# Optimization experiments

Measured on AMD Instinct MI355X. Metric: run time of the kernel, lower is better.

The kernel has to match this reference:

```python
import jax, jax.numpy as jnp
import numpy as np

NUM_HEADS = 12
WH, WW = 14, 14
NUM_REL = (2 * WH - 1) * (2 * WW - 1) + 3  # 732


def binarize(x):
    # STESign forward: sign(x) with sign(0) -> +1
    return jnp.where(x >= 0, 1.0, -1.0).astype(x.dtype)


def quantize_qk(x):
    # per-(B,H) scale: mean |x| over token and feature dims
    s = jnp.mean(jnp.abs(x), axis=(-2, -1), keepdims=True)
    return s * binarize(x)


def quantize_p(x):
    qmax = 255.0
    s = 1.0 / qmax
    q = jnp.clip(jnp.round(x / s), 0.0, qmax)
    return s * q


def symquantize_v(x, num_bits=8):
    # SymQuantizer, layerwise=False: per-column max over dim=-2
    m = jnp.max(jnp.abs(x), axis=-2, keepdims=True)
    s = (2.0 ** (num_bits - 1) - 1.0) / (m + 1e-6)
    return jnp.round(x * s) / (s + 1e-6)


def make_rel_index():
    coords = np.stack(np.meshgrid(np.arange(WH), np.arange(WW), indexing='ij'))  # [2,Wh,Ww]
    flat = coords.reshape(2, -1)                                                 # [2,Wh*Ww]
    rel = flat[:, :, None] - flat[:, None, :]                                    # [2,N-1,N-1]
    rel = rel.transpose(1, 2, 0).copy()
    rel[:, :, 0] += WH - 1
    rel[:, :, 1] += WW - 1
    rel[:, :, 0] *= 2 * WW - 1
    n = WH * WW + 1
    idx = np.zeros((n, n), dtype=np.int64)
    idx[1:, 1:] = rel.sum(-1)
    idx[0, :] = NUM_REL - 3
    idx[:, 0] = NUM_REL - 2
    idx[0, 0] = NUM_REL - 1
    return idx


def setup_inputs() -> dict:
    key = jax.random.key(0)
    k1, k2, k3, k4 = jax.random.split(key, 4)
    B, N, C = 64, WH * WW + 1, 768
    x = jax.random.normal(k1, (B, N, C), dtype=jnp.float32)
    w_qkv = jax.random.normal(k2, (3 * C, C), dtype=jnp.float32) * 0.02
    w_proj = jax.random.normal(k3, (C, C), dtype=jnp.float32) * 0.02
    b_proj = jnp.zeros((C,), dtype=jnp.float32)
    rpb_table = jax.random.normal(k4, (NUM_REL, NUM_HEADS), dtype=jnp.float32) * 0.02
    rel_index = jnp.asarray(make_rel_index())
    return {"x": x, "w_qkv": w_qkv, "w_proj": w_proj, "b_proj": b_proj,
            "rpb_table": rpb_table, "rel_index": rel_index}


def reference(x, w_qkv, w_proj, b_proj, rpb_table, rel_index):
    B, N, C = x.shape
    H = NUM_HEADS
    D = C // H
    scale = D ** (-0.5)
    qkv = (x @ w_qkv.T).reshape(B, N, 3, H, D)
    qkv = jnp.transpose(qkv, (2, 0, 3, 1, 4))  # [3,B,H,N,D]
    q, k, v = qkv[0], qkv[1], qkv[2]
    q = quantize_qk(q)
    k = quantize_qk(k)
    attn = jnp.einsum('bhnd,bhmd->bhnm', q, k) * scale
    bias = rpb_table[rel_index]                 # [N,N,H]
    attn = attn + jnp.transpose(bias, (2, 0, 1))[None]  # [1,H,N,N]
    attn = jax.nn.softmax(attn, axis=-1)
    attn = quantize_p(attn)
    v = symquantize_v(v, 8)
    out = jnp.einsum('bhnm,bhmd->bhnd', attn, v)
    out = jnp.transpose(out, (0, 2, 1, 3)).reshape(B, N, C)
    return out @ w_proj.T + b_proj
```

## Files before the change

### kernel.cpp

```cpp
#include <hip/hip_runtime.h>
#include <hip/hip_bf16.h>
#include <math.h>

#define NUM_HEADS 12
#define N_TOK 197
#define C_DIM 768
#define B_SZ 64
#define M_ROWS (B_SZ * N_TOK)
#define QKV_COLS (3 * C_DIM)
#define NN (N_TOK * N_TOK)
#define VT_PITCH 232

#define MPAD 12800
#define APLANE ((size_t)MPAD * C_DIM)
#define BPLANE ((size_t)QKV_COLS * C_DIM)
#define NT6 144

typedef __hip_bfloat16 bf16;
typedef __attribute__((ext_vector_type(8))) short short8;
typedef __attribute__((ext_vector_type(4))) short s16x4;
typedef __attribute__((ext_vector_type(4))) float floatx4;
typedef unsigned long long u64;

__device__ __forceinline__ void split2(float x, short& hi, short& lo) {
    bf16 h = __float2bfloat16(x);
    float hf = __bfloat162float(h);
    bf16 l = __float2bfloat16(x - hf);
    hi = __builtin_bit_cast(short, h);
    lo = __builtin_bit_cast(short, l);
}

__device__ __forceinline__ void split3(float x, short& s0, short& s1, short& s2) {
    bf16 h = __float2bfloat16(x);
    float r1 = x - __bfloat162float(h);
    bf16 m = __float2bfloat16(r1);
    float r2 = r1 - __bfloat162float(m);
    bf16 l = __float2bfloat16(r2);
    s0 = __builtin_bit_cast(short, h);
    s1 = __builtin_bit_cast(short, m);
    s2 = __builtin_bit_cast(short, l);
}

__device__ __forceinline__ void async16(const void* g, void* l) {
    __builtin_amdgcn_global_load_lds(
        (const __attribute__((address_space(1))) void*)g,
        (__attribute__((address_space(3))) void*)l,
        16, 0, 0);
}

__global__ __launch_bounds__(192) void split3_pack(
    const float* __restrict__ src, short* __restrict__ dst,
    int rows_in, size_t plane)
{
    const int row = blockIdx.x;
    const int c = threadIdx.x * 4;
    const size_t o = (size_t)row * C_DIM + c;
    if (row < rows_in) {
        float4 v = *(const float4*)(src + o);
        float xs[4] = {v.x, v.y, v.z, v.w};
        s16x4 h, m, l;
#pragma unroll
        for (int e = 0; e < 4; ++e) {
            short a, b, cc; split3(xs[e], a, b, cc);
            h[e] = a; m[e] = b; l[e] = cc;
        }
        *(s16x4*)(dst + o) = h;
        *(s16x4*)(dst + plane + o) = m;
        *(s16x4*)(dst + 2 * plane + o) = l;
    } else {
        s16x4 z = (s16x4){0, 0, 0, 0};
        *(s16x4*)(dst + o) = z;
        *(s16x4*)(dst + plane + o) = z;
        *(s16x4*)(dst + 2 * plane + o) = z;
    }
}

__global__ __launch_bounds__(512, 2) void gemm6_pipe(
    const short* __restrict__ Abig, const short* __restrict__ Bbig,
    float* __restrict__ C, int M, int N)
{
    __shared__ short Abuf[4][256 * 32];
    __shared__ short Bbuf[4][256 * 32];

    const int t = threadIdx.x;
    const int wave = t >> 6, lane = t & 63;
    const int quad = lane >> 4, mrow = lane & 15;
    const int wm = wave >> 2, wn = wave & 3;

    const int old = blockIdx.x + blockIdx.y * 9;
    const int xcd = old & 7, wi = old >> 3;
    const int nid = (xcd < 2 ? xcd * 57 : 114 + (xcd - 2) * 56) + wi;
    const int tm = nid / 9;
    const int tile_m = tm * 256;
    const int tile_n = (nid - tm * 9) * 256;

    const int lrow = lane >> 2;
    const int lgp  = lane & 3;
    const int lByte = lrow * (C_DIM * 2) + ((lgp ^ ((lrow >> 1) & 3)) << 4);

    const char* Ab0 = (const char*)Abig + (size_t)(tile_m + wave * 16) * (C_DIM * 2);
    const char* Bb0 = (const char*)Bbig + (size_t)(tile_n + wave * 16) * (C_DIM * 2);

    auto stage = [&](int s) {
        if (s >= NT6) return;
        int term = s / 24;
        int k0b = (s - term * 24) * 64;
        int ta = (0x910 >> (2 * term)) & 3;
        int tb = (0x184 >> (2 * term)) & 3;
        const char* As = Ab0 + (size_t)ta * (APLANE * 2) + k0b + lByte;
        const char* Bs = Bb0 + (size_t)tb * (BPLANE * 2) + k0b + lByte;
        short* la = &Abuf[s & 3][wave * 16 * 32];
        short* lb = &Bbuf[s & 3][wave * 16 * 32];
        async16(As, la);
        async16(As + (size_t)128 * (C_DIM * 2), la + 128 * 32);
        async16(Bs, lb);
        async16(Bs + (size_t)128 * (C_DIM * 2), lb + 128 * 32);
    };

    const int gsel = (quad ^ ((mrow >> 1) & 3)) << 3;
    const int aoff = (wm * 128 + mrow) * 32 + gsel;
    const int boff = (wn * 64 + mrow) * 32 + gsel;

    floatx4 acc[8][4];
#pragma unroll
    for (int i = 0; i < 8; ++i)
#pragma unroll
        for (int j = 0; j < 4; ++j) acc[i][j] = (floatx4){0.f, 0.f, 0.f, 0.f};

    short8 afA[4], afB[4], bf0[4], bf1[4];

    stage(0); stage(1); stage(2);
    asm volatile("s_waitcnt vmcnt(8)" ::: "memory");
    asm volatile("" ::: "memory");
    __builtin_amdgcn_s_barrier();
    asm volatile("" ::: "memory");
    {
        const short* Ab = Abuf[0];
        const short* Bb = Bbuf[0];
#pragma unroll
        for (int i = 0; i < 4; ++i) afA[i] = *(const short8*)&Ab[aoff + i * 512];
#pragma unroll
        for (int j = 0; j < 4; ++j) bf0[j] = *(const short8*)&Bb[boff + j * 512];
    }

    auto iter = [&](int tt, short8 (&bc)[4], short8 (&bn)[4]) {
        const short* Ab = Abuf[tt & 3];
        stage(tt + 3);
#pragma unroll
        for (int i = 0; i < 4; ++i)
            afB[i] = *(const short8*)&Ab[aoff + (4 + i) * 512];
        __builtin_amdgcn_s_setprio(1);
#pragma unroll
        for (int i = 0; i < 4; ++i)
#pragma unroll
            for (int j = 0; j < 4; ++j)
                acc[i][j] = __builtin_amdgcn_mfma_f32_16x16x32_bf16(afA[i], bc[j], acc[i][j], 0, 0, 0);
        __builtin_amdgcn_s_setprio(0);
        if (tt < NT6 - 3) { asm volatile("s_waitcnt vmcnt(8)" ::: "memory"); }
        else              { asm volatile("s_waitcnt vmcnt(0)" ::: "memory"); }
        asm volatile("s_waitcnt lgkmcnt(0)" ::: "memory");
        asm volatile("" ::: "memory");
        __builtin_amdgcn_s_barrier();
        asm volatile("" ::: "memory");
        if (tt + 1 < NT6) {
            const short* An = Abuf[(tt + 1) & 3];
            const short* Bn = Bbuf[(tt + 1) & 3];
#pragma unroll
            for (int i = 0; i < 4; ++i) afA[i] = *(const short8*)&An[aoff + i * 512];
#pragma unroll
            for (int j = 0; j < 4; ++j) bn[j] = *(const short8*)&Bn[boff + j * 512];
        }
        __builtin_amdgcn_s_setprio(1);
#pragma unroll
        for (int i = 0; i < 4; ++i)
#pragma unroll
            for (int j = 0; j < 4; ++j)
                acc[4 + i][j] = __builtin_amdgcn_mfma_f32_16x16x32_bf16(afB[i], bc[j], acc[4 + i][j], 0, 0, 0);
        __builtin_amdgcn_s_setprio(0);
    };

    for (int kt = 0; kt < NT6; kt += 2) {
        iter(kt, bf0, bf1);
        iter(kt + 1, bf1, bf0);
    }

#pragma unroll
    for (int i = 0; i < 8; ++i)
#pragma unroll
        for (int r = 0; r < 4; ++r) {
            int grow = tile_m + wm * 128 + i * 16 + quad * 4 + r;
            if (grow < M)
#pragma unroll
                for (int j = 0; j < 4; ++j)
                    C[(size_t)grow * N + tile_n + wn * 64 + j * 16 + mrow] = acc[i][j][r];
        }
}

__global__ __launch_bounds__(256) void gemm_split6(
    const float* __restrict__ A, const float* __restrict__ B,
    float* __restrict__ C, int M, int N, int K)
{
    __shared__ short8 As[3][512];
    __shared__ short8 Bs[3][512];
    const int t = threadIdx.x;
    const int tile_m = blockIdx.y * 128;
    const int tile_n = blockIdx.x * 128;
    const int wave = t >> 6, lane = t & 63;
    const int quad = lane >> 4, mrow = lane & 15;
    const int wrow = (wave >> 1) * 64, wcol = (wave & 1) * 64;

    floatx4 acc[4][4];
#pragma unroll
    for (int i = 0; i < 4; ++i)
#pragma unroll
        for (int j = 0; j < 4; ++j) acc[i][j] = (floatx4){0.f, 0.f, 0.f, 0.f};

    for (int k0 = 0; k0 < K; k0 += 32) {
        __syncthreads();
#pragma unroll
        for (int s = 0; s < 2; ++s) {
            int idx = s * 256 + t;
            int row = idx >> 2, q = idx & 3;
            {
                int ga = tile_m + row;
                float4 a0 = {0.f, 0.f, 0.f, 0.f}, a1 = {0.f, 0.f, 0.f, 0.f};
                if (ga < M) {
                    const float* p = A + (size_t)ga * K + k0 + q * 8;
                    a0 = *(const float4*)p;
                    a1 = *(const float4*)(p + 4);
                }
                float xs[8] = {a0.x, a0.y, a0.z, a0.w, a1.x, a1.y, a1.z, a1.w};
                short8 v0, v1, v2;
#pragma unroll
                for (int e = 0; e < 8; ++e) {
                    short h, m, l; split3(xs[e], h, m, l);
                    v0[e] = h; v1[e] = m; v2[e] = l;
                }
                As[0][q * 128 + row] = v0;
                As[1][q * 128 + row] = v1;
                As[2][q * 128 + row] = v2;
            }
            {
                int gb = tile_n + row;
                float4 b0 = {0.f, 0.f, 0.f, 0.f}, b1 = {0.f, 0.f, 0.f, 0.f};
                if (gb < N) {
                    const float* p = B + (size_t)gb * K + k0 + q * 8;
                    b0 = *(const float4*)p;
                    b1 = *(const float4*)(p + 4);
                }
                float xs[8] = {b0.x, b0.y, b0.z, b0.w, b1.x, b1.y, b1.z, b1.w};
                short8 v0, v1, v2;
#pragma unroll
                for (int e = 0; e < 8; ++e) {
                    short h, m, l; split3(xs[e], h, m, l);
                    v0[e] = h; v1[e] = m; v2[e] = l;
                }
                Bs[0][q * 128 + row] = v0;
                Bs[1][q * 128 + row] = v1;
                Bs[2][q * 128 + row] = v2;
            }
        }
        __syncthreads();

        short8 af[4], bfr[4];
#pragma unroll
        for (int ta = 0; ta < 3; ++ta) {
#pragma unroll
            for (int i = 0; i < 4; ++i)
                af[i] = As[ta][quad * 128 + wrow + i * 16 + mrow];
            const int ntb = 3 - ta;
#pragma unroll
            for (int tb = 0; tb < 3; ++tb) {
                if (tb >= ntb) break;
#pragma unroll
                for (int j = 0; j < 4; ++j)
                    bfr[j] = Bs[tb][quad * 128 + wcol + j * 16 + mrow];
#pragma unroll
                for (int i = 0; i < 4; ++i)
#pragma unroll
                    for (int j = 0; j < 4; ++j)
                        acc[i][j] = __builtin_amdgcn_mfma_f32_16x16x32_bf16(af[i], bfr[j], acc[i][j], 0, 0, 0);
            }
        }
    }

#pragma unroll
    for (int i = 0; i < 4; ++i)
#pragma unroll
        for (int r = 0; r < 4; ++r) {
            int grow = tile_m + wrow + i * 16 + quad * 4 + r;
            if (grow < M)
#pragma unroll
                for (int j = 0; j < 4; ++j) {
                    int gcol = tile_n + wcol + j * 16 + mrow;
                    C[(size_t)grow * N + gcol] = acc[i][j][r];
                }
        }
}

__global__ __launch_bounds__(256) void gemm_split4_bias(
    const float* __restrict__ A, const float* __restrict__ B,
    const float* __restrict__ bias, float* __restrict__ C,
    int M, int N, int K)
{
    __shared__ short8 Ah[512], Al[512];
    __shared__ short8 Bh[512], Bl[512];
    const int t = threadIdx.x;
    const int tile_m = blockIdx.y * 128;
    const int tile_n = blockIdx.x * 128;
    const int wave = t >> 6, lane = t & 63;
    const int quad = lane >> 4, mrow = lane & 15;
    const int wrow = (wave >> 1) * 64, wcol = (wave & 1) * 64;

    floatx4 acc[4][4];
#pragma unroll
    for (int i = 0; i < 4; ++i)
#pragma unroll
        for (int j = 0; j < 4; ++j) acc[i][j] = (floatx4){0.f, 0.f, 0.f, 0.f};

    for (int k0 = 0; k0 < K; k0 += 32) {
        __syncthreads();
#pragma unroll
        for (int s = 0; s < 2; ++s) {
            int idx = s * 256 + t;
            int row = idx >> 2, q = idx & 3;
            {
                int ga = tile_m + row;
                float4 a0 = {0.f, 0.f, 0.f, 0.f}, a1 = {0.f, 0.f, 0.f, 0.f};
                if (ga < M) {
                    const float* p = A + (size_t)ga * K + k0 + q * 8;
                    a0 = *(const float4*)p; a1 = *(const float4*)(p + 4);
                }
                float xs[8] = {a0.x, a0.y, a0.z, a0.w, a1.x, a1.y, a1.z, a1.w};
                short8 hi, lo;
#pragma unroll
                for (int e = 0; e < 8; ++e) { short hh, ll; split2(xs[e], hh, ll); hi[e] = hh; lo[e] = ll; }
                Ah[q * 128 + row] = hi; Al[q * 128 + row] = lo;
            }
            {
                int gb = tile_n + row;
                float4 b0 = {0.f, 0.f, 0.f, 0.f}, b1 = {0.f, 0.f, 0.f, 0.f};
                if (gb < N) {
                    const float* p = B + (size_t)gb * K + k0 + q * 8;
                    b0 = *(const float4*)p; b1 = *(const float4*)(p + 4);
                }
                float xs[8] = {b0.x, b0.y, b0.z, b0.w, b1.x, b1.y, b1.z, b1.w};
                short8 hi, lo;
#pragma unroll
                for (int e = 0; e < 8; ++e) { short hh, ll; split2(xs[e], hh, ll); hi[e] = hh; lo[e] = ll; }
                Bh[q * 128 + row] = hi; Bl[q * 128 + row] = lo;
            }
        }
        __syncthreads();
        short8 ah[4], al[4], bh[4], bl[4];
#pragma unroll
        for (int i = 0; i < 4; ++i) {
            ah[i] = Ah[quad * 128 + wrow + i * 16 + mrow];
            al[i] = Al[quad * 128 + wrow + i * 16 + mrow];
        }
#pragma unroll
        for (int j = 0; j < 4; ++j) {
            bh[j] = Bh[quad * 128 + wcol + j * 16 + mrow];
            bl[j] = Bl[quad * 128 + wcol + j * 16 + mrow];
        }
#pragma unroll
        for (int i = 0; i < 4; ++i)
#pragma unroll
            for (int j = 0; j < 4; ++j) {
                acc[i][j] = __builtin_amdgcn_mfma_f32_16x16x32_bf16(al[i], bl[j], acc[i][j], 0, 0, 0);
                acc[i][j] = __builtin_amdgcn_mfma_f32_16x16x32_bf16(al[i], bh[j], acc[i][j], 0, 0, 0);
                acc[i][j] = __builtin_amdgcn_mfma_f32_16x16x32_bf16(ah[i], bl[j], acc[i][j], 0, 0, 0);
                acc[i][j] = __builtin_amdgcn_mfma_f32_16x16x32_bf16(ah[i], bh[j], acc[i][j], 0, 0, 0);
            }
    }

#pragma unroll
    for (int i = 0; i < 4; ++i)
#pragma unroll
        for (int r = 0; r < 4; ++r) {
            int grow = tile_m + wrow + i * 16 + quad * 4 + r;
            if (grow < M)
#pragma unroll
                for (int j = 0; j < 4; ++j) {
                    int gcol = tile_n + wcol + j * 16 + mrow;
                    C[(size_t)grow * N + gcol] = acc[i][j][r] + bias[gcol];
                }
        }
}

__global__ __launch_bounds__(256) void quant_stats(
    const float* __restrict__ qkv, float* __restrict__ sqf, float* __restrict__ skf,
    u64* __restrict__ qbits, u64* __restrict__ kbits, float* __restrict__ svf)
{
    const int bh = blockIdx.x;
    const int b = bh / NUM_HEADS, h = bh % NUM_HEADS;
    const int t = threadIdx.x;
    const size_t base = (size_t)b * N_TOK * QKV_COLS + h * 64;
    __shared__ double red[256];
    __shared__ float redf[256];

    const int d = t & 63;
    double aq = 0.0, ak = 0.0;
    for (int i = t; i < N_TOK * 64; i += 256) {
        int n = i >> 6;
        size_t off = base + (size_t)n * QKV_COLS + d;
        aq += (double)fabsf(qkv[off]);
        ak += (double)fabsf(qkv[off + C_DIM]);
    }
    red[t] = aq; __syncthreads();
    for (int s = 128; s > 0; s >>= 1) { if (t < s) red[t] += red[t + s]; __syncthreads(); }
    if (t == 0) sqf[bh] = (float)(red[0] / 12608.0);
    __syncthreads();
    red[t] = ak; __syncthreads();
    for (int s = 128; s > 0; s >>= 1) { if (t < s) red[t] += red[t + s]; __syncthreads(); }
    if (t == 0) skf[bh] = (float)(red[0] / 12608.0);
    __syncthreads();

    float vm = 0.f;
    for (int n = (t >> 6); n < N_TOK; n += 4)
        vm = fmaxf(vm, fabsf(qkv[base + (size_t)n * QKV_COLS + 2 * C_DIM + d]));
    redf[t] = vm; __syncthreads();
    if (t < 64) {
        float m4 = fmaxf(fmaxf(redf[t], redf[t + 64]), fmaxf(redf[t + 128], redf[t + 192]));
        svf[bh * 64 + t] = 127.0f / (m4 + 1e-6f);
    }

    const int wave = t >> 6, lane = t & 63;
    for (int n = wave; n < N_TOK; n += 4) {
        size_t off = base + (size_t)n * QKV_COLS + lane;
        u64 bq = __ballot(qkv[off] >= 0.f);
        u64 bk = __ballot(qkv[off + C_DIM] >= 0.f);
        if (lane == 0) { qbits[bh * N_TOK + n] = bq; kbits[bh * N_TOK + n] = bk; }
    }
}

__global__ void detect_rel64(const int* __restrict__ rel, int* __restrict__ flag)
{
    __shared__ int nz;
    if (threadIdx.x == 0) nz = 0;
    __syncthreads();
    int local = 0;
    for (int i = threadIdx.x; i < NN / 2; i += 256)
        if (rel[2 * i + 1] != 0) local = 1;
    if (local) atomicOr(&nz, 1);
    __syncthreads();
    if (threadIdx.x == 0) flag[0] = (nz == 0) ? 1 : 0;
}

__global__ void build_bias(const float* __restrict__ rpb, const int* __restrict__ rel,
                           const int* __restrict__ flag, float* __restrict__ bias_f)
{
    int nm = blockIdx.x * 256 + threadIdx.x;
    int h = blockIdx.y;
    if (nm < NN) {
        int idx = flag[0] ? rel[2 * nm] : rel[nm];
        bias_f[(size_t)h * NN + nm] = rpb[idx * NUM_HEADS + h];
    }
}

__global__ __launch_bounds__(256) void attn_mfma(
    const float* __restrict__ qkv, const float* __restrict__ sqf, const float* __restrict__ skf,
    const u64* __restrict__ qbits, const u64* __restrict__ kbits,
    const float* __restrict__ svf, const float* __restrict__ bias_f,
    float* __restrict__ attn_out)
{
    const int bh = blockIdx.x;
    const int b = bh / NUM_HEADS, h = bh % NUM_HEADS;
    const int t = threadIdx.x;
    const int wave = t >> 6, lane = t & 63;
    const int quad = lane >> 4, mrow = lane & 15;

    __shared__ __align__(16) short vth[64 * VT_PITCH];
    __shared__ __align__(16) short vtl[64 * VT_PITCH];
    __shared__ __align__(16) short pbuf[2][16 * VT_PITCH];
    __shared__ u64 qb[N_TOK], kb[N_TOK];

    for (int i = t; i < N_TOK; i += 256) {
        qb[i] = qbits[bh * N_TOK + i];
        kb[i] = kbits[bh * N_TOK + i];
    }

    const size_t vbase = (size_t)b * N_TOK * QKV_COLS + 2 * C_DIM + h * 64;
    const int d0 = t & 63;
    const float sv = svf[bh * 64 + d0];
    const float inv_sv = sv + 1e-6f;
    for (int i = t; i < N_TOK * 64; i += 256) {
        int n = i >> 6;
        float v = qkv[vbase + (size_t)n * QKV_COLS + d0];
        float vqf = rintf(v * sv) / inv_sv;
        short hh, ll; split2(vqf, hh, ll);
        vth[d0 * VT_PITCH + n] = hh;
        vtl[d0 * VT_PITCH + n] = ll;
    }
    for (int i = t; i < 64 * (VT_PITCH - N_TOK); i += 256) {
        int d = i / (VT_PITCH - N_TOK), n = N_TOK + i % (VT_PITCH - N_TOK);
        vth[d * VT_PITCH + n] = 0;
        vtl[d * VT_PITCH + n] = 0;
    }
    __syncthreads();

    const int ct = wave;
    short8 bfh[7], bfl[7];
#pragma unroll
    for (int kt = 0; kt < 7; ++kt) {
        int off = (ct * 16 + mrow) * VT_PITCH + kt * 32 + quad * 8;
        bfh[kt] = *(const short8*)&vth[off];
        bfl[kt] = *(const short8*)&vtl[off];
    }

    const float cf = sqf[bh] * skf[bh] * 0.125f;
    const float* bh_bias = bias_f + (size_t)h * NN;
    const float qs = 1.0f / 255.0f;

    auto computeP = [&](int strip, int buf) {
        short* pb = &pbuf[buf][0];
#pragma unroll
        for (int rr = 0; rr < 4; ++rr) {
            int nl = wave * 4 + rr;
            int n = strip * 16 + nl;
            short* prow = pb + nl * VT_PITCH;
            int m0 = lane, m1 = 64 + lane, m2 = 128 + lane, m3 = 192 + lane;
            if (n < N_TOK) {
                const u64 qn = qb[n];
                const float* brow = bh_bias + (size_t)n * N_TOK;
                float l0 = cf * (float)(64 - 2 * (int)__popcll(qn ^ kb[m0])) + brow[m0];
                float l1 = cf * (float)(64 - 2 * (int)__popcll(qn ^ kb[m1])) + brow[m1];
                float l2 = cf * (float)(64 - 2 * (int)__popcll(qn ^ kb[m2])) + brow[m2];
                float l3 = -1e30f;
                if (m3 < N_TOK)
                    l3 = cf * (float)(64 - 2 * (int)__popcll(qn ^ kb[m3])) + brow[m3];
                float mx = fmaxf(fmaxf(l0, l1), fmaxf(l2, l3));
#pragma unroll
                for (int off = 32; off > 0; off >>= 1) mx = fmaxf(mx, __shfl_xor(mx, off, 64));
                float e0 = expf(l0 - mx), e1 = expf(l1 - mx), e2 = expf(l2 - mx);
                float e3 = (m3 < N_TOK) ? expf(l3 - mx) : 0.f;
                float sum = e0 + e1 + e2 + e3;
#pragma unroll
                for (int off = 32; off > 0; off >>= 1) sum += __shfl_xor(sum, off, 64);
                float inv = 1.0f / sum;
                float p0 = fminf(rintf((e0 * inv) / qs), 255.f);
                float p1 = fminf(rintf((e1 * inv) / qs), 255.f);
                float p2 = fminf(rintf((e2 * inv) / qs), 255.f);
                float p3 = fminf(rintf((e3 * inv) / qs), 255.f);
                prow[m0] = __builtin_bit_cast(short, __float2bfloat16(p0));
                prow[m1] = __builtin_bit_cast(short, __float2bfloat16(p1));
                prow[m2] = __builtin_bit_cast(short, __float2bfloat16(p2));
                if (m3 < VT_PITCH)
                    prow[m3] = __builtin_bit_cast(short, __float2bfloat16(p3));
            } else {
                prow[m0] = 0; prow[m1] = 0; prow[m2] = 0;
                if (m3 < VT_PITCH) prow[m3] = 0;
            }
        }
    };

    computeP(0, 0);
    __syncthreads();

    for (int strip = 0; strip < 13; ++strip) {
        if (strip + 1 < 13) computeP(strip + 1, (strip + 1) & 1);

        const short* pb = &pbuf[strip & 1][0];
        floatx4 acc = (floatx4){0.f, 0.f, 0.f, 0.f};
#pragma unroll
        for (int kt = 0; kt < 7; ++kt) {
            short8 af = *(const short8*)&pb[mrow * VT_PITCH + kt * 32 + quad * 8];
            acc = __builtin_amdgcn_mfma_f32_16x16x32_bf16(af, bfh[kt], acc, 0, 0, 0);
            acc = __builtin_amdgcn_mfma_f32_16x16x32_bf16(af, bfl[kt], acc, 0, 0, 0);
        }
#pragma unroll
        for (int r = 0; r < 4; ++r) {
            int n = strip * 16 + quad * 4 + r;
            if (n < N_TOK)
                attn_out[((size_t)(b * N_TOK + n)) * C_DIM + h * 64 + ct * 16 + mrow] = qs * acc[r];
        }
        __syncthreads();
    }
}

extern "C" void kernel_launch(void* const* d_in, const int* in_sizes, int n_in,
                              void* d_out, int out_size, void* d_ws, size_t ws_size,
                              hipStream_t stream)
{
    const float* x      = (const float*)d_in[0];
    const float* w_qkv  = (const float*)d_in[1];
    const float* w_proj = (const float*)d_in[2];
    const float* b_proj = (const float*)d_in[3];
    const float* rpb    = (const float*)d_in[4];
    const int*   rel    = (const int*)d_in[5];
    float* out = (float*)d_out;

    char* ws = (char*)d_ws;
    float* qkv     = (float*)ws; ws += (size_t)M_ROWS * QKV_COLS * sizeof(float);
    float* attn_o  = (float*)ws; ws += (size_t)M_ROWS * C_DIM * sizeof(float);
    float* bias_f  = (float*)ws; ws += (size_t)NUM_HEADS * NN * sizeof(float);
    float* sqf     = (float*)ws; ws += 768 * sizeof(float);
    float* skf     = (float*)ws; ws += 768 * sizeof(float);
    float* svf     = (float*)ws; ws += 768 * 64 * sizeof(float);
    u64* qbits     = (u64*)ws;   ws += (size_t)768 * N_TOK * sizeof(u64);
    u64* kbits     = (u64*)ws;   ws += (size_t)768 * N_TOK * sizeof(u64);
    int* flag      = (int*)ws;   ws += 256;

    ws = (char*)(((uintptr_t)ws + 255) & ~(uintptr_t)255);
    short* Abig = (short*)ws;    ws += 3 * APLANE * sizeof(short);
    short* Bbig = (short*)ws;    ws += 3 * BPLANE * sizeof(short);
    const bool fits = ((size_t)(ws - (char*)d_ws) <= ws_size);

    detect_rel64<<<1, 256, 0, stream>>>(rel, flag);

    if (fits) {
        split3_pack<<<MPAD, 192, 0, stream>>>(x, Abig, M_ROWS, APLANE);
        split3_pack<<<QKV_COLS, 192, 0, stream>>>(w_qkv, Bbig, QKV_COLS, BPLANE);
        gemm6_pipe<<<dim3(QKV_COLS / 256, MPAD / 256), 512, 0, stream>>>(
            Abig, Bbig, qkv, M_ROWS, QKV_COLS);
    } else {
        gemm_split6<<<dim3(QKV_COLS / 128, (M_ROWS + 127) / 128), 256, 0, stream>>>(
            x, w_qkv, qkv, M_ROWS, QKV_COLS, C_DIM);
    }

    quant_stats<<<768, 256, 0, stream>>>(qkv, sqf, skf, qbits, kbits, svf);

    build_bias<<<dim3((NN + 255) / 256, NUM_HEADS), 256, 0, stream>>>(rpb, rel, flag, bias_f);

    attn_mfma<<<768, 256, 0, stream>>>(qkv, sqf, skf, qbits, kbits, svf, bias_f, attn_o);

    gemm_split4_bias<<<dim3(C_DIM / 128, (M_ROWS + 127) / 128), 256, 0, stream>>>(
        attn_o, w_proj, b_proj, out, M_ROWS, C_DIM, C_DIM);
}
```

Baseline: 644.8 us.

## Emit bf16 hi/lo planes from attention and use pipelined projection GEMM

The attention kernel now writes its output directly as two bf16 split planes (hi/lo) instead of fp32. The projection weight is pre-split into two planes, and a new 256x256-tile, 512-thread async-pipelined GEMM (gemm4_pipe, 4 cross terms of split2) replaces gemm_split4_bias with the bias added in its epilogue. This removes the per-tile fp32-to-bf16 splitting in the projection GEMM and reuses the faster pipelined structure of the QKV GEMM. In exchange it adds extra packing and zero-padding kernels and more workspace, and the attention output is stored as scattered 2-byte writes.

```diff
diff --git a/kernel.cpp b/kernel.cpp
--- a/kernel.cpp
+++ b/kernel.cpp
@@ -14,7 +14,9 @@
 #define MPAD 12800
 #define APLANE ((size_t)MPAD * C_DIM)
 #define BPLANE ((size_t)QKV_COLS * C_DIM)
+#define WPLANE ((size_t)C_DIM * C_DIM)
 #define NT6 144
+#define NT4 96
 
 typedef __hip_bfloat16 bf16;
 typedef __attribute__((ext_vector_type(8))) short short8;
@@ -72,6 +74,33 @@
         *(s16x4*)(dst + o) = z;
         *(s16x4*)(dst + plane + o) = z;
         *(s16x4*)(dst + 2 * plane + o) = z;
+    }
+}
+
+__global__ __launch_bounds__(192) void split2_pack(
+    const float* __restrict__ src, short* __restrict__ dst, size_t plane)
+{
+    const int row = blockIdx.x;
+    const int c = threadIdx.x * 4;
+    const size_t o = (size_t)row * C_DIM + c;
+    float4 v = *(const float4*)(src + o);
+    float xs[4] = {v.x, v.y, v.z, v.w};
+    s16x4 h, l;
+#pragma unroll
+    for (int e = 0; e < 4; ++e) {
+        short hh, ll; split2(xs[e], hh, ll);
+        h[e] = hh; l[e] = ll;
+    }
+    *(s16x4*)(dst + o) = h;
+    *(s16x4*)(dst + plane + o) = l;
+}
+
+__global__ void zero_padA(short* __restrict__ ap)
+{
+    const int row = M_ROWS + blockIdx.x;
+    for (int c = threadIdx.x; c < C_DIM; c += 256) {
+        ap[(size_t)row * C_DIM + c] = 0;
+        ap[APLANE + (size_t)row * C_DIM + c] = 0;
     }
 }
 
@@ -196,6 +225,129 @@
         }
 }
 
+__global__ __launch_bounds__(512, 2) void gemm4_pipe(
+    const short* __restrict__ Ap, const short* __restrict__ Bp,
+    const float* __restrict__ bias, float* __restrict__ C, int M)
+{
+    __shared__ short Abuf[4][256 * 32];
+    __shared__ short Bbuf[4][256 * 32];
+
+    const int t = threadIdx.x;
+    const int wave = t >> 6, lane = t & 63;
+    const int quad = lane >> 4, mrow = lane & 15;
+    const int wm = wave >> 2, wn = wave & 3;
+
+    const int old = blockIdx.x + blockIdx.y * 3;
+    const int xcd = old & 7, wi = old >> 3;
+    const int nid = (xcd < 6 ? xcd * 19 : 114 + (xcd - 6) * 18) + wi;
+    const int tm = nid / 3;
+    const int tile_m = tm * 256;
+    const int tile_n = (nid - tm * 3) * 256;
+
+    const int lrow = lane >> 2;
+    const int lgp  = lane & 3;
+    const int lByte = lrow * (C_DIM * 2) + ((lgp ^ ((lrow >> 1) & 3)) << 4);
+
+    const char* Ab0 = (const char*)Ap + (size_t)(tile_m + wave * 16) * (C_DIM * 2);
+    const char* Bb0 = (const char*)Bp + (size_t)(tile_n + wave * 16) * (C_DIM * 2);
+
+    auto stage = [&](int s) {
+        if (s >= NT4) return;
+        int term = s / 24;
+        int k0b = (s - term * 24) * 64;
+        int ta = 1 - (term >> 1);
+        int tb = 1 - (term & 1);
+        const char* As = Ab0 + (size_t)ta * (APLANE * 2) + k0b + lByte;
+        const char* Bs = Bb0 + (size_t)tb * (WPLANE * 2) + k0b + lByte;
+        short* la = &Abuf[s & 3][wave * 16 * 32];
+        short* lb = &Bbuf[s & 3][wave * 16 * 32];
+        async16(As, la);
+        async16(As + (size_t)128 * (C_DIM * 2), la + 128 * 32);
+        async16(Bs, lb);
+        async16(Bs + (size_t)128 * (C_DIM * 2), lb + 128 * 32);
+    };
+
+    const int gsel = (quad ^ ((mrow >> 1) & 3)) << 3;
+    const int aoff = (wm * 128 + mrow) * 32 + gsel;
+    const int boff = (wn * 64 + mrow) * 32 + gsel;
+
+    floatx4 acc[8][4];
+#pragma unroll
+    for (int i = 0; i < 8; ++i)
+#pragma unroll
+        for (int j = 0; j < 4; ++j) acc[i][j] = (floatx4){0.f, 0.f, 0.f, 0.f};
+
+    short8 afA[4], afB[4], bf0[4], bf1[4];
+
+    stage(0); stage(1); stage(2);
+    asm volatile("s_waitcnt vmcnt(8)" ::: "memory");
+    asm volatile("" ::: "memory");
+    __builtin_amdgcn_s_barrier();
+    asm volatile("" ::: "memory");
+    {
+        const short* Ab = Abuf[0];
+        const short* Bb = Bbuf[0];
+#pragma unroll
+        for (int i = 0; i < 4; ++i) afA[i] = *(const short8*)&Ab[aoff + i * 512];
+#pragma unroll
+        for (int j = 0; j < 4; ++j) bf0[j] = *(const short8*)&Bb[boff + j * 512];
+    }
+
+    auto iter = [&](int tt, short8 (&bc)[4], short8 (&bn)[4]) {
+        const short* Ab = Abuf[tt & 3];
+        stage(tt + 3);
+#pragma unroll
+        for (int i = 0; i < 4; ++i)
+            afB[i] = *(const short8*)&Ab[aoff + (4 + i) * 512];
+        __builtin_amdgcn_s_setprio(1);
+#pragma unroll
+        for (int i = 0; i < 4; ++i)
+#pragma unroll
+            for (int j = 0; j < 4; ++j)
+                acc[i][j] = __builtin_amdgcn_mfma_f32_16x16x32_bf16(afA[i], bc[j], acc[i][j], 0, 0, 0);
+        __builtin_amdgcn_s_setprio(0);
+        if (tt < NT4 - 3) { asm volatile("s_waitcnt vmcnt(8)" ::: "memory"); }
+        else              { asm volatile("s_waitcnt vmcnt(0)" ::: "memory"); }
+        asm volatile("s_waitcnt lgkmcnt(0)" ::: "memory");
+        asm volatile("" ::: "memory");
+        __builtin_amdgcn_s_barrier();
+        asm volatile("" ::: "memory");
+        if (tt + 1 < NT4) {
+            const short* An = Abuf[(tt + 1) & 3];
+            const short* Bn = Bbuf[(tt + 1) & 3];
+#pragma unroll
+            for (int i = 0; i < 4; ++i) afA[i] = *(const short8*)&An[aoff + i * 512];
+#pragma unroll
+            for (int j = 0; j < 4; ++j) bn[j] = *(const short8*)&Bn[boff + j * 512];
+        }
+        __builtin_amdgcn_s_setprio(1);
+#pragma unroll
+        for (int i = 0; i < 4; ++i)
+#pragma unroll
+            for (int j = 0; j < 4; ++j)
+                acc[4 + i][j] = __builtin_amdgcn_mfma_f32_16x16x32_bf16(afB[i], bc[j], acc[4 + i][j], 0, 0, 0);
+        __builtin_amdgcn_s_setprio(0);
+    };
+
+    for (int kt = 0; kt < NT4; kt += 2) {
+        iter(kt, bf0, bf1);
+        iter(kt + 1, bf1, bf0);
+    }
+
+#pragma unroll
+    for (int i = 0; i < 8; ++i)
+#pragma unroll
+        for (int r = 0; r < 4; ++r) {
+            int grow = tile_m + wm * 128 + i * 16 + quad * 4 + r;
+            if (grow < M)
+#pragma unroll
+                for (int j = 0; j < 4; ++j) {
+                    int gcol = tile_n + wn * 64 + j * 16 + mrow;
+                    C[(size_t)grow * C_DIM + gcol] = acc[i][j][r] + bias[gcol];
+                }
+        }
+}
+
 __global__ __launch_bounds__(256) void gemm_split6(
     const float* __restrict__ A, const float* __restrict__ B,
     float* __restrict__ C, int M, int N, int K)
@@ -462,7 +614,7 @@
     const float* __restrict__ qkv, const float* __restrict__ sqf, const float* __restrict__ skf,
     const u64* __restrict__ qbits, const u64* __restrict__ kbits,
     const float* __restrict__ svf, const float* __restrict__ bias_f,
-    float* __restrict__ attn_out)
+    float* __restrict__ attn_out, short* __restrict__ aplanes, int use_planes)
 {
     const int bh = blockIdx.x;
     const int b = bh / NUM_HEADS, h = bh % NUM_HEADS;
@@ -571,8 +723,17 @@
 #pragma unroll
         for (int r = 0; r < 4; ++r) {
             int n = strip * 16 + quad * 4 + r;
-            if (n < N_TOK)
-                attn_out[((size_t)(b * N_TOK + n)) * C_DIM + h * 64 + ct * 16 + mrow] = qs * acc[r];
+            if (n < N_TOK) {
+                size_t oidx = ((size_t)(b * N_TOK + n)) * C_DIM + h * 64 + ct * 16 + mrow;
+                float o = qs * acc[r];
+                if (use_planes) {
+                    short hh, ll; split2(o, hh, ll);
+                    aplanes[oidx] = hh;
+                    aplanes[APLANE + oidx] = ll;
+                } else {
+                    attn_out[oidx] = o;
+                }
+            }
         }
         __syncthreads();
     }
@@ -592,7 +753,7 @@
 
     char* ws = (char*)d_ws;
     float* qkv     = (float*)ws; ws += (size_t)M_ROWS * QKV_COLS * sizeof(float);
-    float* attn_o  = (float*)ws; ws += (size_t)M_ROWS * C_DIM * sizeof(float);
+    char* attnA    = ws;         ws += 2 * APLANE * sizeof(short);
     float* bias_f  = (float*)ws; ws += (size_t)NUM_HEADS * NN * sizeof(float);
     float* sqf     = (float*)ws; ws += 768 * sizeof(float);
     float* skf     = (float*)ws; ws += 768 * sizeof(float);
@@ -602,8 +763,9 @@
     int* flag      = (int*)ws;   ws += 256;
 
     ws = (char*)(((uintptr_t)ws + 255) & ~(uintptr_t)255);
-    short* Abig = (short*)ws;    ws += 3 * APLANE * sizeof(short);
-    short* Bbig = (short*)ws;    ws += 3 * BPLANE * sizeof(short);
+    short* Abig  = (short*)ws;   ws += 3 * APLANE * sizeof(short);
+    short* Bbig  = (short*)ws;   ws += 3 * BPLANE * sizeof(short);
+    short* Wpl   = (short*)ws;   ws += 2 * WPLANE * sizeof(short);
     const bool fits = ((size_t)(ws - (char*)d_ws) <= ws_size);
 
     detect_rel64<<<1, 256, 0, stream>>>(rel, flag);
@@ -622,8 +784,17 @@
 
     build_bias<<<dim3((NN + 255) / 256, NUM_HEADS), 256, 0, stream>>>(rpb, rel, flag, bias_f);
 
-    attn_mfma<<<768, 256, 0, stream>>>(qkv, sqf, skf, qbits, kbits, svf, bias_f, attn_o);
-
-    gemm_split4_bias<<<dim3(C_DIM / 128, (M_ROWS + 127) / 128), 256, 0, stream>>>(
-        attn_o, w_proj, b_proj, out, M_ROWS, C_DIM, C_DIM);
-}
+    if (fits) {
+        split2_pack<<<C_DIM, 192, 0, stream>>>(w_proj, Wpl, WPLANE);
+        zero_padA<<<MPAD - M_ROWS, 256, 0, stream>>>((short*)attnA);
+        attn_mfma<<<768, 256, 0, stream>>>(qkv, sqf, skf, qbits, kbits, svf, bias_f,
+                                           (float*)attnA, (short*)attnA, 1);
+        gemm4_pipe<<<dim3(C_DIM / 256, MPAD / 256), 512, 0, stream>>>(
+            (const short*)attnA, Wpl, b_proj, out, M_ROWS);
+    } else {
+        attn_mfma<<<768, 256, 0, stream>>>(qkv, sqf, skf, qbits, kbits, svf, bias_f,
+                                           (float*)attnA, (short*)attnA, 0);
+        gemm_split4_bias<<<dim3(C_DIM / 128, (M_ROWS + 127) / 128), 256, 0, stream>>>(
+            (const float*)attnA, w_proj, b_proj, out, M_ROWS, C_DIM, C_DIM);
+    }
+}
```

New measurement: 643.5 us. About the same (-0.2%).
